# Kernel optimization log

Measured on AMD Instinct MI355X. Metric: run time of the kernel, lower is better.

## Reference

```python
import jax, jax.numpy as jnp
import numpy as np

C = 256          # channels
K_SIZE = 3       # involution kernel size
GROUPS = 16      # groups g
HIDDEN = C // 4  # reduction_ratio = 4
B, H, W = 8, 64, 64


def setup_inputs() -> dict:
    key = jax.random.key(0)
    k0, k1, k2 = jax.random.split(key, 3)
    kk = K_SIZE * K_SIZE
    return {
        "x": jax.random.normal(k0, (B, C, H, W), dtype=jnp.float32),
        # 1x1 conv weights stored as matrices [out_ch, in_ch]
        "w_reduce": jax.random.normal(k1, (HIDDEN, C), dtype=jnp.float32) * 0.05,
        "b_reduce": jnp.zeros((HIDDEN,), dtype=jnp.float32),
        "w_span": jax.random.normal(k2, (GROUPS * kk, HIDDEN), dtype=jnp.float32) * 0.05,
        "b_span": jnp.zeros((GROUPS * kk,), dtype=jnp.float32),
    }


def reference(x, w_reduce, b_reduce, w_span, b_span):
    b, c, h, w = x.shape
    k, g = K_SIZE, GROUPS
    kk = k * k
    # stride == 1 -> sigma is identity; kernel generator: 1x1 conv -> relu -> 1x1 conv
    hid = jax.nn.relu(jnp.einsum('oc,bcxy->boxy', w_reduce, x)
                      + b_reduce[None, :, None, None])
    Kmap = (jnp.einsum('oc,bcxy->boxy', w_span, hid)
            + b_span[None, :, None, None])            # [B, g*kk, H, W]
    Kmap = Kmap.reshape(b, g, kk, h, w)
    # unfold with padding k//2, stride 1: extract k*k shifted views
    pad = k // 2
    xp = jnp.pad(x, ((0, 0), (0, 0), (pad, pad), (pad, pad)))
    patches = jnp.stack(
        [xp[:, :, i:i + h, j:j + w] for i in range(k) for j in range(k)],
        axis=2)                                        # [B, C, kk, H, W]
    patches = patches.reshape(b, g, c // g, kk, h, w)
    # location-specific, channel-agnostic multiply-reduce over kk
    out = jnp.einsum('bgnkhw,bgkhw->bgnhw', patches, Kmap)
    return out.reshape(b, c, h, w)
```

## Files before the change

### kernel.cpp

```cpp
#include <hip/hip_runtime.h>

#define CCH   256
#define HIDN  64
#define GK    144
#define NB    8
#define NHW   4096
#define NG    16
#define CPG   16

#define W1T_OFF  0
#define W2T_OFF  16384
#define KMAP_OFF 25600

__global__ __launch_bounds__(256) void wtrans_kernel(
    const float* __restrict__ w_reduce, const float* __restrict__ w_span,
    float* __restrict__ ws)
{
    const int idx = blockIdx.x * 256 + threadIdx.x;
    if (idx < 16384) {
        const int c = idx >> 6, o = idx & 63;
        ws[W1T_OFF + idx] = w_reduce[o * CCH + c];
    } else {
        const int i2 = idx - 16384;
        const int o = i2 / 144, j = i2 - o * 144;
        ws[W2T_OFF + i2] = w_span[j * HIDN + o];
    }
}

__global__ __launch_bounds__(512, 4) void gen_kernel(
    const float* __restrict__ x,
    const float* __restrict__ b_reduce,
    const float* __restrict__ b_span,
    const float* __restrict__ ws_ro,
    float* __restrict__ kmap)
{
    __shared__ float smem[16384];
    float (*xs)[64] = (float (*)[64])smem;

    const float* __restrict__ w1T = ws_ro + W1T_OFF;
    const float* __restrict__ w2T = ws_ro + W2T_OFF;

    const int lane = threadIdx.x & 63;
    const int wid  = __builtin_amdgcn_readfirstlane(threadIdx.x >> 6);

    const int row = blockIdx.x;
    const int b   = row >> 6;
    const int hr  = row & 63;

    const float* xb = x + (size_t)b * (CCH * NHW) + hr * 64;

    {
        const int cl = lane >> 4;
        const int p4 = (lane & 15) * 4;
        #pragma unroll
        for (int t = 0; t < 8; ++t) {
            const int c0 = wid * 32 + t * 4;
            const float* src = xb + (size_t)(c0 + cl) * NHW + p4;
            __builtin_amdgcn_global_load_lds(
                (const __attribute__((address_space(1))) unsigned int*)src,
                (__attribute__((address_space(3))) unsigned int*)&xs[c0][0],
                16, 0, 0);
        }
    }
    __syncthreads();

    const int o0 = wid * 8;
    float acc[8];
    #pragma unroll
    for (int i = 0; i < 8; ++i) acc[i] = b_reduce[o0 + i];

    #pragma unroll 8
    for (int c = 0; c < CCH; ++c) {
        const float xv = xs[c][lane];
        const float* w1c = w1T + c * HIDN + o0;
        #pragma unroll
        for (int i = 0; i < 8; ++i)
            acc[i] = fmaf(w1c[i], xv, acc[i]);
    }
    __syncthreads();

    float (*hid)[65] = (float (*)[65])smem;
    #pragma unroll
    for (int i = 0; i < 8; ++i) hid[lane][o0 + i] = fmaxf(acc[i], 0.0f);
    __syncthreads();

    const int j0 = wid * 18;
    float kv[18];
    #pragma unroll
    for (int jj = 0; jj < 18; ++jj) kv[jj] = b_span[j0 + jj];

    #pragma unroll 4
    for (int o = 0; o < HIDN; ++o) {
        const float hv = hid[lane][o];
        const float* w2o = w2T + o * GK + j0;
        #pragma unroll
        for (int jj = 0; jj < 18; ++jj)
            kv[jj] = fmaf(w2o[jj], hv, kv[jj]);
    }

    const bool vwm = (lane > 0), vwp = (lane < 63);
    const bool vhm = (hr  > 0), vhp = (hr  < 63);
    const bool vk[9] = { vhm && vwm, vhm, vhm && vwp,
                         vwm,        true, vwp,
                         vhp && vwm, vhp, vhp && vwp };

    float* kout = kmap + (size_t)b * (GK * NHW) + hr * 64 + lane;
    #pragma unroll
    for (int jj = 0; jj < 18; ++jj)
        kout[(size_t)(j0 + jj) * NHW] = vk[jj % 9] ? kv[jj] : 0.0f;
}

__global__ __launch_bounds__(256) void apply_kernel(
    const float* __restrict__ x,
    const float* __restrict__ kmap,
    float* __restrict__ out)
{
    const int t  = blockIdx.x * 256 + threadIdx.x;
    const int hw = t & 4095;
    const int bg = t >> 12;
    const int g  = bg & 15;
    const int b  = bg >> 4;
    const int h  = hw >> 6;
    const int w  = hw & 63;

    const float* kp = kmap + ((size_t)b * GK + g * 9) * NHW + hw;
    float kv[9];
    int   off[9];
    #pragma unroll
    for (int di = 0; di < 3; ++di) {
        const int hh  = h + di - 1;
        const int hcl = min(max(hh, 0), 63);
        #pragma unroll
        for (int dj = 0; dj < 3; ++dj) {
            const int ww  = w + dj - 1;
            const int wcl = min(max(ww, 0), 63);
            const int k   = di * 3 + dj;
            kv[k]  = kp[k * NHW];
            off[k] = (hcl - h) * 64 + (wcl - w);
        }
    }

    const float* xp = x   + ((size_t)b * CCH + g * CPG) * NHW + hw;
    float*       op = out + ((size_t)b * CCH + g * CPG) * NHW + hw;

    #pragma unroll 4
    for (int n = 0; n < CPG; ++n) {
        float acc = 0.0f;
        #pragma unroll
        for (int k = 0; k < 9; ++k)
            acc = fmaf(xp[n * NHW + off[k]], kv[k], acc);
        op[n * NHW] = acc;
    }
}

extern "C" void kernel_launch(void* const* d_in, const int* in_sizes, int n_in,
                              void* d_out, int out_size, void* d_ws, size_t ws_size,
                              hipStream_t stream) {
    const float* x        = (const float*)d_in[0];
    const float* w_reduce = (const float*)d_in[1];
    const float* b_reduce = (const float*)d_in[2];
    const float* w_span   = (const float*)d_in[3];
    const float* b_span   = (const float*)d_in[4];
    float* out = (float*)d_out;
    float* ws  = (float*)d_ws;

    float* kmap = ws + KMAP_OFF;

    wtrans_kernel<<<dim3(100), dim3(256), 0, stream>>>(w_reduce, w_span, ws);
    gen_kernel<<<dim3(NB * 64), dim3(512), 0, stream>>>(
        x, b_reduce, b_span, ws, kmap);
    apply_kernel<<<dim3(NB * NG * NHW / 256), dim3(256), 0, stream>>>(
        x, kmap, out);
}
```

Measured before the change: 126.0 us.

## Fuse kernel generation and involution apply into one kernel

Merges the kernel-map generator and the apply pass into a single kernel. Each block computes the 144 kernel weights for its row in registers and applies them straight to its 32 channels per wave, so the kernel map is never written to or read back from global memory and one launch is dropped. It also transposes the hidden buffer in LDS so reads go along lanes, and swizzles the block index so consecutive blocks land on different batches. The apply step now reads neighbouring x values from global memory (mostly cache hits), with parallelism limited to 512 blocks.

```diff
diff --git a/kernel.cpp b/kernel.cpp
--- a/kernel.cpp
+++ b/kernel.cpp
@@ -5,12 +5,9 @@
 #define GK    144
 #define NB    8
 #define NHW   4096
-#define NG    16
-#define CPG   16
 
 #define W1T_OFF  0
 #define W2T_OFF  16384
-#define KMAP_OFF 25600
 
 __global__ __launch_bounds__(256) void wtrans_kernel(
     const float* __restrict__ w_reduce, const float* __restrict__ w_span,
@@ -27,12 +24,12 @@
     }
 }
 
-__global__ __launch_bounds__(512, 4) void gen_kernel(
+__global__ __launch_bounds__(512, 4) void invol_fused(
     const float* __restrict__ x,
     const float* __restrict__ b_reduce,
     const float* __restrict__ b_span,
     const float* __restrict__ ws_ro,
-    float* __restrict__ kmap)
+    float* __restrict__ out)
 {
     __shared__ float smem[16384];
     float (*xs)[64] = (float (*)[64])smem;
@@ -43,7 +40,8 @@
     const int lane = threadIdx.x & 63;
     const int wid  = __builtin_amdgcn_readfirstlane(threadIdx.x >> 6);
 
-    const int row = blockIdx.x;
+    const int raw = blockIdx.x;
+    const int row = ((raw & 7) << 6) | (raw >> 3);
     const int b   = row >> 6;
     const int hr  = row & 63;
 
@@ -79,9 +77,9 @@
     }
     __syncthreads();
 
-    float (*hid)[65] = (float (*)[65])smem;
+    float (*hid)[64] = (float (*)[64])smem;
     #pragma unroll
-    for (int i = 0; i < 8; ++i) hid[lane][o0 + i] = fmaxf(acc[i], 0.0f);
+    for (int i = 0; i < 8; ++i) hid[o0 + i][lane] = fmaxf(acc[i], 0.0f);
     __syncthreads();
 
     const int j0 = wid * 18;
@@ -91,7 +89,7 @@
 
     #pragma unroll 4
     for (int o = 0; o < HIDN; ++o) {
-        const float hv = hid[lane][o];
+        const float hv = hid[o][lane];
         const float* w2o = w2T + o * GK + j0;
         #pragma unroll
         for (int jj = 0; jj < 18; ++jj)
@@ -103,53 +101,29 @@
     const bool vk[9] = { vhm && vwm, vhm, vhm && vwp,
                          vwm,        true, vwp,
                          vhp && vwm, vhp, vhp && vwp };
-
-    float* kout = kmap + (size_t)b * (GK * NHW) + hr * 64 + lane;
     #pragma unroll
     for (int jj = 0; jj < 18; ++jj)
-        kout[(size_t)(j0 + jj) * NHW] = vk[jj % 9] ? kv[jj] : 0.0f;
-}
+        kv[jj] = vk[jj % 9] ? kv[jj] : 0.0f;
 
-__global__ __launch_bounds__(256) void apply_kernel(
-    const float* __restrict__ x,
-    const float* __restrict__ kmap,
-    float* __restrict__ out)
-{
-    const int t  = blockIdx.x * 256 + threadIdx.x;
-    const int hw = t & 4095;
-    const int bg = t >> 12;
-    const int g  = bg & 15;
-    const int b  = bg >> 4;
-    const int h  = hw >> 6;
-    const int w  = hw & 63;
+    const int oWm = vwm ? -1  : 0, oWp = vwp ? 1  : 0;
+    const int oHm = vhm ? -64 : 0, oHp = vhp ? 64 : 0;
+    const int oo[9] = { oHm + oWm, oHm, oHm + oWp,
+                        oWm,       0,   oWp,
+                        oHp + oWm, oHp, oHp + oWp };
 
-    const float* kp = kmap + ((size_t)b * GK + g * 9) * NHW + hw;
-    float kv[9];
-    int   off[9];
-    #pragma unroll
-    for (int di = 0; di < 3; ++di) {
-        const int hh  = h + di - 1;
-        const int hcl = min(max(hh, 0), 63);
-        #pragma unroll
-        for (int dj = 0; dj < 3; ++dj) {
-            const int ww  = w + dj - 1;
-            const int wcl = min(max(ww, 0), 63);
-            const int k   = di * 3 + dj;
-            kv[k]  = kp[k * NHW];
-            off[k] = (hcl - h) * 64 + (wcl - w);
-        }
-    }
-
-    const float* xp = x   + ((size_t)b * CCH + g * CPG) * NHW + hw;
-    float*       op = out + ((size_t)b * CCH + g * CPG) * NHW + hw;
+    const float* xrow = xb + lane;
+    float*       orow = out + (size_t)b * (CCH * NHW) + hr * 64 + lane;
 
     #pragma unroll 4
-    for (int n = 0; n < CPG; ++n) {
-        float acc = 0.0f;
+    for (int m = 0; m < 32; ++m) {
+        const int c  = wid * 32 + m;
+        const int gl = m >> 4;
+        const float* xc = xrow + (size_t)c * NHW;
+        float a = 0.0f;
         #pragma unroll
         for (int k = 0; k < 9; ++k)
-            acc = fmaf(xp[n * NHW + off[k]], kv[k], acc);
-        op[n * NHW] = acc;
+            a = fmaf(xc[oo[k]], kv[gl * 9 + k], a);
+        orow[(size_t)c * NHW] = a;
     }
 }
 
@@ -164,11 +138,7 @@
     float* out = (float*)d_out;
     float* ws  = (float*)d_ws;
 
-    float* kmap = ws + KMAP_OFF;
-
     wtrans_kernel<<<dim3(100), dim3(256), 0, stream>>>(w_reduce, w_span, ws);
-    gen_kernel<<<dim3(NB * 64), dim3(512), 0, stream>>>(
-        x, b_reduce, b_span, ws, kmap);
-    apply_kernel<<<dim3(NB * NG * NHW / 256), dim3(256), 0, stream>>>(
-        x, kmap, out);
+    invol_fused<<<dim3(NB * 64), dim3(512), 0, stream>>>(
+        x, b_reduce, b_span, ws, out);
 }
```

Measured after the change: 121.4 us. 1.04x faster.
